# Kernel tuning notes

Measured on AMD Instinct MI355X. Metric: run time of the kernel, lower is better.

The kernel has to match this reference:

```python
import jax, jax.numpy as jnp
import numpy as np

S, T, C, L_GNN, L_TF, H = 8, 16, 128, 3, 2, 4
B = 512
FF = 4 * C
EPS = 1e-5


def setup_inputs() -> dict:
    key = jax.random.key(0)
    ks = jax.random.split(key, 24)
    w = lambda k, shape: jax.random.normal(k, shape, jnp.float32) * 0.05
    inp = {}
    inp["xx"] = jax.random.randint(ks[0], (B, T, S, S, S), 0, 3, dtype=jnp.int32)
    inp["ss"] = jax.random.uniform(ks[1], (B, 1), jnp.float32)
    # DynamicGNNv2 params
    inp["Win"] = w(ks[2], (C, 5)); inp["b_in"] = w(ks[3], (C,))
    inp["Wl"] = w(ks[4], (L_GNN, C, C)); inp["bl"] = w(ks[5], (L_GNN, C))   # SAGEConv lin_l (neighbors)
    inp["Wr"] = w(ks[6], (L_GNN, C, C))                                      # SAGEConv lin_r (root, no bias)
    inp["ln_g"] = jnp.ones((C,), jnp.float32); inp["ln_b"] = jnp.zeros((C,), jnp.float32)  # shared LayerNorm
    # TransformerEncoder params (norm_first, relu, dropout=0 at eval)
    inp["Wqkv"] = w(ks[7], (L_TF, 3 * C, C)); inp["bqkv"] = w(ks[8], (L_TF, 3 * C))
    inp["Wo"] = w(ks[9], (L_TF, C, C)); inp["bo"] = w(ks[10], (L_TF, C))
    inp["ln1_g"] = jnp.ones((L_TF, C), jnp.float32); inp["ln1_b"] = jnp.zeros((L_TF, C), jnp.float32)
    inp["ln2_g"] = jnp.ones((L_TF, C), jnp.float32); inp["ln2_b"] = jnp.zeros((L_TF, C), jnp.float32)
    inp["W1"] = w(ks[11], (L_TF, FF, C)); inp["b1"] = w(ks[12], (L_TF, FF))
    inp["W2"] = w(ks[13], (L_TF, C, FF)); inp["b2"] = w(ks[14], (L_TF, C))
    inp["Wact"] = w(ks[15], (C, S ** 3)); inp["bact"] = w(ks[16], (C,))
    inp["Wsc"] = w(ks[17], (C, 1)); inp["bsc"] = w(ks[18], (C,))
    return inp


def layernorm(x, g, b):
    mu = x.mean(-1, keepdims=True)
    var = ((x - mu) ** 2).mean(-1, keepdims=True)
    return (x - mu) * jax.lax.rsqrt(var + EPS) * g + b


def reference(xx, ss, Win, b_in, Wl, bl, Wr, ln_g, ln_b, Wqkv, bqkv, Wo, bo,
              ln1_g, ln1_b, ln2_g, ln2_b, W1, b1, W2, b2, Wact, bact, Wsc, bsc):
    Bc = xx.shape[0]
    S3 = S ** 3
    frame0 = xx[:, 0].reshape(Bc, S3).astype(jnp.float32)            # (B,S^3)
    m = (frame0 != 0).astype(jnp.float32)                            # active-node mask
    grid = jnp.arange(S3)
    i, j, k = grid // (S * S), (grid // S) % S, grid % S
    coord = jnp.stack([i, j, k], -1).astype(jnp.float32) / (S - 1)   # (S^3,3)
    feat = jnp.concatenate([
        jnp.broadcast_to(coord, (Bc, S3, 3)),
        (frame0 / 2.0)[..., None],
        jnp.broadcast_to((ss / S)[:, None, :], (Bc, S3, 1)),
    ], -1)                                                            # (B,S^3,5)
    x = feat @ Win.T + b_in                                           # lin_in
    mm = m[..., None]
    n = m.sum(-1, keepdims=True)[..., None]                           # nodes per graph (B,1,1)
    for l in range(L_GNN):
        # complete graph (no self loops): mean over neighbors = (sum_active - self)/(N-1)
        s = (x * mm).sum(1, keepdims=True)                            # (B,1,C)
        neigh = jnp.where(n > 1, (s - x) / jnp.maximum(n - 1.0, 1.0), 0.0)
        h = neigh @ Wl[l].T + bl[l] + x @ Wr[l].T                     # SAGEConv
        x = layernorm(jax.nn.relu(h), ln_g, ln_b)
    full = x * mm                                                     # scatter-fill into dense (B,S^3,C)
    # pooling matmul: mean over each i/j/k slice -> (B,3S,C)
    poolW = jnp.concatenate([
        (i[None, :] == jnp.arange(S)[:, None]).astype(jnp.float32),
        (j[None, :] == jnp.arange(S)[:, None]).astype(jnp.float32),
        (k[None, :] == jnp.arange(S)[:, None]).astype(jnp.float32),
    ], 0)                                                             # (3S,S^3)
    gnn_emb = jnp.einsum('ps,bsc->bpc', poolW, full) / poolW.sum(1)[None, :, None]
    # transformer over past actions
    a = xx[:, 1:].reshape(Bc, T - 1, S3).astype(jnp.float32) @ Wact.T + bact
    Hd = C // H
    scale = 1.0 / np.sqrt(Hd).astype(np.float32)
    split_heads = lambda t: t.reshape(Bc, -1, H, Hd).transpose(0, 2, 1, 3)
    for l in range(L_TF):
        h1 = layernorm(a, ln1_g[l], ln1_b[l])
        q, kk, v = jnp.split(h1 @ Wqkv[l].T + bqkv[l], 3, axis=-1)
        q, kk, v = split_heads(q), split_heads(kk), split_heads(v)
        att = jax.nn.softmax(jnp.einsum('bhqd,bhkd->bhqk', q, kk) * scale, -1)
        o = jnp.einsum('bhqk,bhkd->bhqd', att, v).transpose(0, 2, 1, 3).reshape(Bc, -1, C)
        a = a + (o @ Wo[l].T + bo[l])
        h2 = layernorm(a, ln2_g[l], ln2_b[l])
        a = a + (jax.nn.relu(h2 @ W1[l].T + b1[l]) @ W2[l].T + b2[l])
    act_emb = a.mean(1)                                               # (B,C)
    mv_emb = jax.nn.relu(ss @ Wsc.T + bsc)                            # (B,C)
    return jnp.concatenate([gnn_emb, act_emb[:, None], mv_emb[:, None]], 1)  # (B,3S+2,C)
```

## Files before the change

### kernel.cpp

```cpp
#include <hip/hip_runtime.h>
#include <hip/hip_bf16.h>
#include <string.h>

typedef __hip_bfloat16 bf16;
typedef __attribute__((ext_vector_type(8))) short short8;
typedef __attribute__((ext_vector_type(4))) float f32x4;

#define Bsz 512
#define S3  512
#define Tsz 16
#define Cc  128
#define TT  15
#define EPSv 1e-5f

__device__ __forceinline__ float u2f(unsigned short u) {
    return __uint_as_float(((unsigned)u) << 16);
}
__device__ __forceinline__ float ulo(unsigned u) { return __uint_as_float(u << 16); }
__device__ __forceinline__ float uhi(unsigned u) { return __uint_as_float(u & 0xffff0000u); }
__device__ __forceinline__ unsigned short f2bu(float v) {
    bf16 h = __float2bfloat16(v);
    unsigned short u; memcpy(&u, &h, 2); return u;
}
__device__ __forceinline__ unsigned short bfr16(float a) {
    unsigned u = __float_as_uint(a);
    u = u + 0x7fffu + ((u >> 16) & 1u);
    return (unsigned short)(u >> 16);
}
__device__ __forceinline__ unsigned fpack2(float a, float b) {
    unsigned ua = __float_as_uint(a), ub = __float_as_uint(b);
    ua = ua + 0x7fffu + ((ua >> 16) & 1u);
    ub = ub + 0x7fffu + ((ub >> 16) & 1u);
    return (ua >> 16) | (ub & 0xffff0000u);
}
__device__ __forceinline__ float dot4(float4 a, float4 b) {
    return a.x*b.x + a.y*b.y + a.z*b.z + a.w*b.w;
}

__global__ __launch_bounds__(256) void k_tpack(const float* __restrict__ src,
                                               float* __restrict__ dst,
                                               int NR, int NK)
{
    __shared__ float tile[32][33];
    int k0 = blockIdx.x * 32, r0 = blockIdx.y * 32;
    int lr = threadIdx.x >> 5, lk = threadIdx.x & 31;
    for (int i = lr; i < 32; i += 8)
        tile[i][lk] = src[(size_t)(r0 + i) * NK + k0 + lk];
    __syncthreads();
    int c = threadIdx.x & 31, k4 = threadIdx.x >> 5;
    float4 v;
    v.x = tile[c][k4 * 4 + 0]; v.y = tile[c][k4 * 4 + 1];
    v.z = tile[c][k4 * 4 + 2]; v.w = tile[c][k4 * 4 + 3];
    ((float4*)dst)[(size_t)(k0 / 4 + k4) * NR + r0 + c] = v;
}

__global__ __launch_bounds__(256) void k_cvt5(
    const float* __restrict__ s0, const float* __restrict__ s1,
    const float* __restrict__ s2, const float* __restrict__ s3,
    const float* __restrict__ s4, ushort* __restrict__ dst)
{
    int i = blockIdx.x * 256 + threadIdx.x;
    if (i >= 114688) return;
    const float* src; int rel;
    if (i < 16384)      { src = s0; rel = i; }
    else if (i < 40960) { src = s1; rel = i - 16384; }
    else if (i < 49152) { src = s2; rel = i - 40960; }
    else if (i < 81920) { src = s3; rel = i - 49152; }
    else                { src = s4; rel = i - 81920; }
    float4 v = ((const float4*)src)[rel];
    ushort4 o;
    o.x = f2bu(v.x); o.y = f2bu(v.y); o.z = f2bu(v.z); o.w = f2bu(v.w);
    ((ushort4*)dst)[i] = o;
}

__global__ __launch_bounds__(256) void k_dwall(
    const int* __restrict__ xx, const float* __restrict__ Wl,
    const float* __restrict__ Wr, ushort* __restrict__ dbuf)
{
    __shared__ float pc[4];
    __shared__ float winv;
    int b = blockIdx.x, l = blockIdx.y, tid = threadIdx.x;
    const int* x0 = xx + (size_t)b * Tsz * S3;
    int c = (x0[tid] != 0) + (x0[tid + 256] != 0);
    for (int off = 32; off; off >>= 1) c += __shfl_xor(c, off, 64);
    if ((tid & 63) == 0) pc[tid >> 6] = (float)c;
    __syncthreads();
    if (tid == 0) {
        float n = pc[0] + pc[1] + pc[2] + pc[3];
        winv = (n > 1.f) ? 1.f / (n - 1.f) : 0.f;
    }
    __syncthreads();
    float inv = winv;
    const float* wl = Wl + l * 16384;
    const float* wr = Wr + l * 16384;
    ushort* dst = dbuf + (size_t)(b * 3 + l) * 32 * 512;
    for (int item = tid; item < 2048; item += 256) {
        int f = item >> 6, lane = item & 63;
        int t = f >> 2, ks = f & 3, ml = lane & 15, q = lane >> 4;
        int n = t * 16 + ml, kb = ks * 32 + q * 8;
        const float4* wlr = (const float4*)(wl + n * 128 + kb);
        const float4* wrr = (const float4*)(wr + n * 128 + kb);
        float4 a0 = wlr[0], a1 = wlr[1];
        float4 r0 = wrr[0], r1 = wrr[1];
        ushort4 o0, o1;
        o0.x = f2bu(r0.x - inv * a0.x); o0.y = f2bu(r0.y - inv * a0.y);
        o0.z = f2bu(r0.z - inv * a0.z); o0.w = f2bu(r0.w - inv * a0.w);
        o1.x = f2bu(r1.x - inv * a1.x); o1.y = f2bu(r1.y - inv * a1.y);
        o1.z = f2bu(r1.z - inv * a1.z); o1.w = f2bu(r1.w - inv * a1.w);
        ushort* dp = dst + (size_t)f * 512 + lane * 8;
        *(ushort4*)dp = o0;
        *(ushort4*)(dp + 4) = o1;
    }
}

__global__ __launch_bounds__(1024) void k_torso(
    const int* __restrict__ xx, const float* __restrict__ ss,
    const float* __restrict__ Win, const float* __restrict__ b_in,
    const ushort* __restrict__ dbuf,
    const float4* __restrict__ WlP, const float* __restrict__ blv,
    const float* __restrict__ lng, const float* __restrict__ lnb,
    float* __restrict__ out)
{
    __shared__ ushort X[512 * 136];
    __shared__ float  mC[512];
    __shared__ float  sred[16 * 128];
    __shared__ float  ssc[128];
    __shared__ float  sbase[128];
    __shared__ float  gln[128], bln[128];
    __shared__ float  scnt[16];
    __shared__ float  invS;

    int b = blockIdx.x, tid = threadIdx.x;
    int wv = tid >> 6, lane = tid & 63;
    int ml = lane & 15, quad = lane >> 4;

    {
        int g = wv, cp = lane;
        int co0 = 2 * cp, co1 = 2 * cp + 1;
        const int* x0 = xx + (size_t)b * Tsz * S3;
        float f4c = ss[b] * (1.0f / 8.0f);
        float a0 = Win[co0*5+0], a1 = Win[co0*5+1], a2 = Win[co0*5+2], a3 = Win[co0*5+3];
        float c0 = Win[co1*5+0], c1 = Win[co1*5+1], c2 = Win[co1*5+2], c3 = Win[co1*5+3];
        float ba = b_in[co0] + f4c * Win[co0*5+4];
        float bc = b_in[co1] + f4c * Win[co1*5+4];
        float sp0 = 0.f, sp1 = 0.f; int cnt = 0;
        for (int node = g; node < S3; node += 16) {
            int f0 = x0[node];
            float m = (f0 != 0) ? 1.f : 0.f;
            float ci = (float)(node >> 6) * (1.f / 7.f);
            float cj = (float)((node >> 3) & 7) * (1.f / 7.f);
            float ck = (float)(node & 7) * (1.f / 7.f);
            float ft = (float)f0 * 0.5f;
            float v0 = ba + ci * a0 + cj * a1 + ck * a2 + ft * a3;
            float v1 = bc + ci * c0 + cj * c1 + ck * c2 + ft * c3;
            ((unsigned*)(X + node * 136))[cp] = fpack2(v0, v1);
            sp0 += v0 * m; sp1 += v1 * m;
            cnt += (f0 != 0);
            if (cp == 0) mC[node] = m;
        }
        sred[g * 128 + co0] = sp0;
        sred[g * 128 + co1] = sp1;
        if (cp == 0) scnt[g] = (float)cnt;
    }
    if (tid < 128) { gln[tid] = lng[tid]; bln[tid] = lnb[tid]; }
    __syncthreads();
    if (tid == 0) {
        float n = 0.f;
#pragma unroll
        for (int g = 0; g < 16; g++) n += scnt[g];
        invS = (n > 1.f) ? 1.f / (n - 1.f) : 0.f;
    }
    __syncthreads();
    if (tid < 128) {
        float s = 0.f;
#pragma unroll
        for (int g = 0; g < 16; g++) s += sred[g * 128 + tid];
        ssc[tid] = s * invS;
    }
    __syncthreads();
    if (tid < 128) {
        float a = blv[tid];
        for (int k4 = 0; k4 < 32; k4++)
            a += dot4(*(const float4*)(ssc + k4 * 4), WlP[k4 * 384 + tid]);
        sbase[tid] = a;
    }
    __syncthreads();

    for (int l = 0; l < 3; l++) {
        f32x4 acc[8][2];
#pragma unroll
        for (int t = 0; t < 8; t++)
#pragma unroll
            for (int m = 0; m < 2; m++) acc[t][m] = (f32x4){0.f, 0.f, 0.f, 0.f};

        const ushort* dL  = dbuf + (size_t)(b * 3 + l) * 32 * 512 + lane * 8;
        const ushort* xr0 = X + (wv * 32 + ml) * 136 + quad * 8;
        const ushort* xr1 = xr0 + 16 * 136;

#pragma unroll
        for (int ks = 0; ks < 4; ks++) {
            short8 a0 = *(const short8*)(xr0 + ks * 32);
            short8 a1 = *(const short8*)(xr1 + ks * 32);
            short8 bg0[4], bg1[4];
#pragma unroll
            for (int t = 0; t < 4; t++)
                bg0[t] = *(const short8*)(dL + (size_t)(t * 4 + ks) * 512);
#pragma unroll
            for (int t = 0; t < 4; t++)
                bg1[t] = *(const short8*)(dL + (size_t)((t + 4) * 4 + ks) * 512);
#pragma unroll
            for (int t = 0; t < 4; t++) {
                acc[t][0] = __builtin_amdgcn_mfma_f32_16x16x32_bf16(a0, bg0[t], acc[t][0], 0, 0, 0);
                acc[t][1] = __builtin_amdgcn_mfma_f32_16x16x32_bf16(a1, bg0[t], acc[t][1], 0, 0, 0);
            }
#pragma unroll
            for (int t = 0; t < 4; t++) {
                acc[t + 4][0] = __builtin_amdgcn_mfma_f32_16x16x32_bf16(a0, bg1[t], acc[t + 4][0], 0, 0, 0);
                acc[t + 4][1] = __builtin_amdgcn_mfma_f32_16x16x32_bf16(a1, bg1[t], acc[t + 4][1], 0, 0, 0);
            }
        }

        float bse[8], gg[8], be[8];
#pragma unroll
        for (int t = 0; t < 8; t++) {
            bse[t] = sbase[t * 16 + ml];
            gg[t]  = gln[t * 16 + ml];
            be[t]  = bln[t * 16 + ml];
        }
        float sp[8];
#pragma unroll
        for (int t = 0; t < 8; t++) sp[t] = 0.f;
        bool last = (l == 2);

#pragma unroll
        for (int m = 0; m < 2; m++) {
#pragma unroll
            for (int r = 0; r < 4; r++) {
                int row = wv * 32 + m * 16 + quad * 4 + r;
                float s = 0.f, q = 0.f;
#pragma unroll
                for (int t = 0; t < 8; t++) {
                    float v = fmaxf(acc[t][m][r] + bse[t], 0.f);
                    acc[t][m][r] = v;
                    s += v; q += v * v;
                }
#pragma unroll
                for (int off = 1; off <= 8; off <<= 1) {
                    s += __shfl_xor(s, off, 64);
                    q += __shfl_xor(q, off, 64);
                }
                float mu = s * (1.f / 128.f);
                float rs = rsqrtf(q * (1.f / 128.f) - mu * mu + EPSv);
                float mrow = mC[row];
#pragma unroll
                for (int t = 0; t < 8; t++) {
                    float y = (acc[t][m][r] - mu) * rs * gg[t] + be[t];
                    if (last) y *= mrow;
                    else sp[t] += y * mrow;
                    X[row * 136 + t * 16 + ml] = bfr16(y);
                }
            }
        }

        if (!last) {
#pragma unroll
            for (int t = 0; t < 8; t++) {
                sp[t] += __shfl_xor(sp[t], 16, 64);
                sp[t] += __shfl_xor(sp[t], 32, 64);
            }
            if (quad == 0) {
#pragma unroll
                for (int t = 0; t < 8; t++) sred[wv * 128 + t * 16 + ml] = sp[t];
            }
            __syncthreads();
            if (tid < 128) {
                float s = 0.f;
#pragma unroll
                for (int g = 0; g < 16; g++) s += sred[g * 128 + tid];
                ssc[tid] = s * invS;
            }
            __syncthreads();
            if (tid < 128) {
                float a = blv[(l + 1) * 128 + tid];
                for (int k4 = 0; k4 < 32; k4++)
                    a += dot4(*(const float4*)(ssc + k4 * 4), WlP[k4 * 384 + (l + 1) * 128 + tid]);
                sbase[tid] = a;
            }
            __syncthreads();
        }
    }
    __syncthreads();

    if (tid < 768) {
        int c4 = tid & 31, p = tid >> 5;
        int axis = p >> 3, idx = p & 7;
        float4 sum = {0.f, 0.f, 0.f, 0.f};
        for (int t = 0; t < 64; t++) {
            int node;
            if (axis == 0)      node = idx * 64 + t;
            else if (axis == 1) node = (t >> 3) * 64 + idx * 8 + (t & 7);
            else                node = t * 8 + idx;
            uint2 pk = *(const uint2*)(X + node * 136 + c4 * 4);
            sum.x += ulo(pk.x);
            sum.y += uhi(pk.x);
            sum.z += ulo(pk.y);
            sum.w += uhi(pk.y);
        }
        float4 o;
        o.x = sum.x * (1.f / 64.f); o.y = sum.y * (1.f / 64.f);
        o.z = sum.z * (1.f / 64.f); o.w = sum.w * (1.f / 64.f);
        *(float4*)(out + (size_t)b * 26 * Cc + p * Cc + c4 * 4) = o;
    }
}

__global__ __launch_bounds__(256) void k_tf3(
    const int* __restrict__ xx, const float* __restrict__ ss,
    const ushort* __restrict__ WactB, const float* __restrict__ bact,
    const ushort* __restrict__ WqkvB, const float* __restrict__ bqkv,
    const ushort* __restrict__ WoB, const float* __restrict__ bo,
    const float* __restrict__ ln1g, const float* __restrict__ ln1b,
    const float* __restrict__ ln2g, const float* __restrict__ ln2b,
    const ushort* __restrict__ W1B, const float* __restrict__ b1v,
    const ushort* __restrict__ W2B, const float* __restrict__ b2v,
    const float* __restrict__ Wsc, const float* __restrict__ bsc,
    float* __restrict__ out)
{
    __shared__ float  As[TT * 132];
    __shared__ ushort Qs[16 * 392];
    __shared__ ushort Ab[16 * 136];
    __shared__ ushort Hs[16 * 136];
    __shared__ ushort Fs[16 * 520];
    __shared__ float  Att[60 * 16];
    __shared__ float  mu_s[TT], rs_s[TT];

    int b = blockIdx.x, tid = threadIdx.x;
    int wv = tid >> 6, lane = tid & 63;
    int ml = lane & 15, quad = lane >> 4;

    const int* xa = xx + (size_t)b * Tsz * S3 + S3;
    for (int f = tid; f < TT * 512; f += 256) {
        int t = f >> 9, s = f & 511;
        Fs[t * 520 + s] = bfr16((float)xa[t * 512 + s]);
    }
    __syncthreads();

    {
        f32x4 acc[2];
#pragma unroll
        for (int i = 0; i < 2; i++) acc[i] = (f32x4){0.f, 0.f, 0.f, 0.f};
        const ushort* ar = Fs + ml * 520 + quad * 8;
        for (int ks = 0; ks < 16; ks++) {
            short8 a = *(const short8*)(ar + ks * 32);
#pragma unroll
            for (int i = 0; i < 2; i++) {
                int n0 = (wv * 2 + i) * 16;
                short8 bfr = *(const short8*)(WactB + (size_t)(n0 + ml) * 512 + quad * 8 + ks * 32);
                acc[i] = __builtin_amdgcn_mfma_f32_16x16x32_bf16(a, bfr, acc[i], 0, 0, 0);
            }
        }
#pragma unroll
        for (int i = 0; i < 2; i++) {
            int col = (wv * 2 + i) * 16 + ml;
            float bb = bact[col];
#pragma unroll
            for (int r = 0; r < 4; r++) {
                int row = quad * 4 + r;
                if (row < TT) As[row * 132 + col] = acc[i][r] + bb;
            }
        }
    }
    __syncthreads();

    for (int l = 0; l < 2; l++) {
        const float* bq  = bqkv + l * 384;
        const float* bol = bo + l * 128;
        const float* g1  = ln1g + l * 128; const float* be1 = ln1b + l * 128;
        const float* g2  = ln2g + l * 128; const float* be2 = ln2b + l * 128;
        const float* b1l = b1v + l * 512;  const float* b2l = b2v + l * 128;

        for (int r = wv; r < TT; r += 4) {
            float2 v = *(const float2*)(As + r * 132 + lane * 2);
            float s = v.x + v.y, q = v.x * v.x + v.y * v.y;
            for (int off = 32; off; off >>= 1) {
                s += __shfl_xor(s, off, 64);
                q += __shfl_xor(q, off, 64);
            }
            if (lane == 0) {
                float mu = s * (1.f / 128.f);
                mu_s[r] = mu;
                rs_s[r] = rsqrtf(q * (1.f / 128.f) - mu * mu + EPSv);
            }
        }
        __syncthreads();
        for (int f = tid; f < TT * 64; f += 256) {
            int t = f >> 6, cp = f & 63;
            float mu = mu_s[t], rs = rs_s[t];
            float x0 = (As[t * 132 + 2 * cp]     - mu) * rs * g1[2 * cp]     + be1[2 * cp];
            float x1 = (As[t * 132 + 2 * cp + 1] - mu) * rs * g1[2 * cp + 1] + be1[2 * cp + 1];
            ((unsigned*)(Ab + t * 136))[cp] = fpack2(x0, x1);
        }
        __syncthreads();

        {
            short8 a[4];
            const ushort* ar = Ab + ml * 136 + quad * 8;
#pragma unroll
            for (int ks = 0; ks < 4; ks++) a[ks] = *(const short8*)(ar + ks * 32);
#pragma unroll
            for (int i = 0; i < 6; i++) {
                int n0 = (wv * 6 + i) * 16;
                f32x4 acc = (f32x4){0.f, 0.f, 0.f, 0.f};
                const ushort* wb = WqkvB + (size_t)(l * 384 + n0 + ml) * 128 + quad * 8;
#pragma unroll
                for (int ks = 0; ks < 4; ks++) {
                    short8 bfr = *(const short8*)(wb + ks * 32);
                    acc = __builtin_amdgcn_mfma_f32_16x16x32_bf16(a[ks], bfr, acc, 0, 0, 0);
                }
                int col = n0 + ml;
                float bb = bq[col];
#pragma unroll
                for (int r = 0; r < 4; r++) {
                    int row = quad * 4 + r;
                    if (row < TT) Qs[row * 392 + col] = bfr16(acc[r] + bb);
                }
            }
        }
        __syncthreads();

        if (tid < 60) {
            int h = tid / 15, tq = tid % 15;
            const ushort* qp = Qs + tq * 392 + h * 32;
            float sc[TT];
            float mx = -1e30f;
#pragma unroll
            for (int tk = 0; tk < TT; tk++) {
                const ushort* kp = Qs + tk * 392 + 128 + h * 32;
                float d = 0.f;
#pragma unroll
                for (int u = 0; u < 32; u += 4) {
                    uint2 qa = *(const uint2*)(qp + u);
                    uint2 ka = *(const uint2*)(kp + u);
                    d += ulo(qa.x) * ulo(ka.x) + uhi(qa.x) * uhi(ka.x)
                       + ulo(qa.y) * ulo(ka.y) + uhi(qa.y) * uhi(ka.y);
                }
                d *= 0.17677669529663689f;
                sc[tk] = d; mx = fmaxf(mx, d);
            }
            float sum = 0.f;
#pragma unroll
            for (int tk = 0; tk < TT; tk++) { float e = __expf(sc[tk] - mx); sc[tk] = e; sum += e; }
            float r = 1.f / sum;
#pragma unroll
            for (int tk = 0; tk < TT; tk++) Att[tid * 16 + tk] = sc[tk] * r;
        }
        __syncthreads();

        for (int f = tid; f < TT * 64; f += 256) {
            int t = f >> 6, cp = f & 63;
            int h = cp >> 4;
            const float* ap = Att + (h * 15 + t) * 16;
            const ushort* vp = Qs + 256 + 2 * cp;
            float a0 = 0.f, a1 = 0.f;
#pragma unroll
            for (int tk = 0; tk < TT; tk++) {
                float w = ap[tk];
                unsigned pk = *(const unsigned*)(vp + tk * 392);
                a0 += w * ulo(pk);
                a1 += w * uhi(pk);
            }
            ((unsigned*)(Hs + t * 136))[cp] = fpack2(a0, a1);
        }
        __syncthreads();

        {
            short8 a[4];
            const ushort* ar = Hs + ml * 136 + quad * 8;
#pragma unroll
            for (int ks = 0; ks < 4; ks++) a[ks] = *(const short8*)(ar + ks * 32);
#pragma unroll
            for (int i = 0; i < 2; i++) {
                int n0 = (wv * 2 + i) * 16;
                f32x4 acc = (f32x4){0.f, 0.f, 0.f, 0.f};
                const ushort* wb = WoB + (size_t)(l * 128 + n0 + ml) * 128 + quad * 8;
#pragma unroll
                for (int ks = 0; ks < 4; ks++) {
                    short8 bfr = *(const short8*)(wb + ks * 32);
                    acc = __builtin_amdgcn_mfma_f32_16x16x32_bf16(a[ks], bfr, acc, 0, 0, 0);
                }
                int col = n0 + ml;
                float bb = bol[col];
#pragma unroll
                for (int r = 0; r < 4; r++) {
                    int row = quad * 4 + r;
                    if (row < TT) As[row * 132 + col] += acc[r] + bb;
                }
            }
        }
        __syncthreads();

        for (int r = wv; r < TT; r += 4) {
            float2 v = *(const float2*)(As + r * 132 + lane * 2);
            float s = v.x + v.y, q = v.x * v.x + v.y * v.y;
            for (int off = 32; off; off >>= 1) {
                s += __shfl_xor(s, off, 64);
                q += __shfl_xor(q, off, 64);
            }
            if (lane == 0) {
                float mu = s * (1.f / 128.f);
                mu_s[r] = mu;
                rs_s[r] = rsqrtf(q * (1.f / 128.f) - mu * mu + EPSv);
            }
        }
        __syncthreads();
        for (int f = tid; f < TT * 64; f += 256) {
            int t = f >> 6, cp = f & 63;
            float mu = mu_s[t], rs = rs_s[t];
            float x0 = (As[t * 132 + 2 * cp]     - mu) * rs * g2[2 * cp]     + be2[2 * cp];
            float x1 = (As[t * 132 + 2 * cp + 1] - mu) * rs * g2[2 * cp + 1] + be2[2 * cp + 1];
            ((unsigned*)(Ab + t * 136))[cp] = fpack2(x0, x1);
        }
        __syncthreads();

        {
            short8 a[4];
            const ushort* ar = Ab + ml * 136 + quad * 8;
#pragma unroll
            for (int ks = 0; ks < 4; ks++) a[ks] = *(const short8*)(ar + ks * 32);
#pragma unroll
            for (int i = 0; i < 8; i++) {
                int n0 = (wv * 8 + i) * 16;
                f32x4 acc = (f32x4){0.f, 0.f, 0.f, 0.f};
                const ushort* wb = W1B + (size_t)(l * 512 + n0 + ml) * 128 + quad * 8;
#pragma unroll
                for (int ks = 0; ks < 4; ks++) {
                    short8 bfr = *(const short8*)(wb + ks * 32);
                    acc = __builtin_amdgcn_mfma_f32_16x16x32_bf16(a[ks], bfr, acc, 0, 0, 0);
                }
                int col = n0 + ml;
                float bb = b1l[col];
#pragma unroll
                for (int r = 0; r < 4; r++) {
                    int row = quad * 4 + r;
                    if (row < TT) Fs[row * 520 + col] = bfr16(fmaxf(acc[r] + bb, 0.f));
                }
            }
        }
        __syncthreads();

        {
            f32x4 acc[2];
#pragma unroll
            for (int i = 0; i < 2; i++) acc[i] = (f32x4){0.f, 0.f, 0.f, 0.f};
            const ushort* ar = Fs + ml * 520 + quad * 8;
            for (int ks = 0; ks < 16; ks++) {
                short8 a = *(const short8*)(ar + ks * 32);
#pragma unroll
                for (int i = 0; i < 2; i++) {
                    int n0 = (wv * 2 + i) * 16;
                    short8 bfr = *(const short8*)(W2B + (size_t)(l * 128 + n0 + ml) * 512 + quad * 8 + ks * 32);
                    acc[i] = __builtin_amdgcn_mfma_f32_16x16x32_bf16(a, bfr, acc[i], 0, 0, 0);
                }
            }
#pragma unroll
            for (int i = 0; i < 2; i++) {
                int col = (wv * 2 + i) * 16 + ml;
                float bb = b2l[col];
#pragma unroll
                for (int r = 0; r < 4; r++) {
                    int row = quad * 4 + r;
                    if (row < TT) As[row * 132 + col] += acc[i][r] + bb;
                }
            }
        }
        __syncthreads();
    }

    if (tid < 128) {
        float s = 0.f;
#pragma unroll
        for (int t = 0; t < TT; t++) s += As[t * 132 + tid];
        out[(size_t)b * 26 * Cc + 24 * Cc + tid] = s * (1.f / 15.f);
    } else if (tid < 256) {
        int co = tid - 128;
        float v = ss[b] * Wsc[co] + bsc[co];
        out[(size_t)b * 26 * Cc + 25 * Cc + co] = fmaxf(v, 0.f);
    }
}

extern "C" void kernel_launch(void* const* d_in, const int* in_sizes, int n_in,
                              void* d_out, int out_size, void* d_ws, size_t ws_size,
                              hipStream_t stream)
{
    (void)in_sizes; (void)n_in; (void)out_size; (void)ws_size;
    const int*   xx   = (const int*)d_in[0];
    const float* ss   = (const float*)d_in[1];
    const float* Win  = (const float*)d_in[2];
    const float* b_in = (const float*)d_in[3];
    const float* Wl   = (const float*)d_in[4];
    const float* bl   = (const float*)d_in[5];
    const float* Wr   = (const float*)d_in[6];
    const float* lng  = (const float*)d_in[7];
    const float* lnb  = (const float*)d_in[8];
    const float* Wqkv = (const float*)d_in[9];
    const float* bqkv = (const float*)d_in[10];
    const float* Wo   = (const float*)d_in[11];
    const float* bo   = (const float*)d_in[12];
    const float* ln1g = (const float*)d_in[13];
    const float* ln1b = (const float*)d_in[14];
    const float* ln2g = (const float*)d_in[15];
    const float* ln2b = (const float*)d_in[16];
    const float* W1   = (const float*)d_in[17];
    const float* b1   = (const float*)d_in[18];
    const float* W2   = (const float*)d_in[19];
    const float* b2   = (const float*)d_in[20];
    const float* Wact = (const float*)d_in[21];
    const float* bact = (const float*)d_in[22];
    const float* Wsc  = (const float*)d_in[23];
    const float* bsc  = (const float*)d_in[24];
    float* out = (float*)d_out;

    char* ws = (char*)d_ws;
    size_t off = 0;
    float* WlT  = (float*)(ws + off); off += 384 * 128 * 4;
    ushort* dbuf  = (ushort*)(ws + off); off += (size_t)Bsz * 3 * 32 * 512 * 2;
    ushort* WactB = (ushort*)(ws + off); off += 128 * 512 * 2;
    ushort* WqkvB = (ushort*)(ws + off); off += 768 * 128 * 2;
    ushort* WoB   = (ushort*)(ws + off); off += 256 * 128 * 2;
    ushort* W1B   = (ushort*)(ws + off); off += 1024 * 128 * 2;
    ushort* W2B   = (ushort*)(ws + off); off += 256 * 512 * 2;

    k_tpack<<<dim3(4, 12), 256, 0, stream>>>(Wl, WlT, 384, 128);
    k_cvt5<<<448, 256, 0, stream>>>(Wact, Wqkv, Wo, W1, W2, WactB);
    k_dwall<<<dim3(Bsz, 3), 256, 0, stream>>>(xx, Wl, Wr, dbuf);

    k_torso<<<Bsz, 1024, 0, stream>>>(xx, ss, Win, b_in, dbuf,
                                      (const float4*)WlT, bl, lng, lnb, out);

    k_tf3<<<Bsz, 256, 0, stream>>>(xx, ss,
                                   WactB, bact, WqkvB, bqkv, WoB, bo,
                                   ln1g, ln1b, ln2g, ln2b,
                                   W1B, b1, W2B, b2,
                                   Wsc, bsc, out);
}
```

Baseline: 316.4 us.

## Replace per-batch combined GNN weights with shared Wl/Wr and dual MFMA accumulation

Previously a kernel built a per-batch bf16 weight matrix (Wr - inv*Wl) for every batch element and layer, writing and then reading about 50 MB of workspace. Now Wl and Wr are converted to bf16 once in six small blocks. The torso kernel runs two sets of MFMAs (root and neighbor) and combines them in the epilogue as accR - inv*accL. This trades doubled MFMA work and extra accumulator registers for far less global memory traffic and better cache reuse of the small shared weights.

```diff
diff --git a/kernel.cpp b/kernel.cpp
--- a/kernel.cpp
+++ b/kernel.cpp
@@ -13,9 +13,6 @@
 #define TT  15
 #define EPSv 1e-5f
 
-__device__ __forceinline__ float u2f(unsigned short u) {
-    return __uint_as_float(((unsigned)u) << 16);
-}
 __device__ __forceinline__ float ulo(unsigned u) { return __uint_as_float(u << 16); }
 __device__ __forceinline__ float uhi(unsigned u) { return __uint_as_float(u & 0xffff0000u); }
 __device__ __forceinline__ unsigned short f2bu(float v) {
@@ -73,40 +70,22 @@
     ((ushort4*)dst)[i] = o;
 }
 
-__global__ __launch_bounds__(256) void k_dwall(
-    const int* __restrict__ xx, const float* __restrict__ Wl,
-    const float* __restrict__ Wr, ushort* __restrict__ dbuf)
+__global__ __launch_bounds__(256) void k_wgnn(
+    const float* __restrict__ Wl, const float* __restrict__ Wr,
+    ushort* __restrict__ wbuf)
 {
-    __shared__ float pc[4];
-    __shared__ float winv;
-    int b = blockIdx.x, l = blockIdx.y, tid = threadIdx.x;
-    const int* x0 = xx + (size_t)b * Tsz * S3;
-    int c = (x0[tid] != 0) + (x0[tid + 256] != 0);
-    for (int off = 32; off; off >>= 1) c += __shfl_xor(c, off, 64);
-    if ((tid & 63) == 0) pc[tid >> 6] = (float)c;
-    __syncthreads();
-    if (tid == 0) {
-        float n = pc[0] + pc[1] + pc[2] + pc[3];
-        winv = (n > 1.f) ? 1.f / (n - 1.f) : 0.f;
-    }
-    __syncthreads();
-    float inv = winv;
-    const float* wl = Wl + l * 16384;
-    const float* wr = Wr + l * 16384;
-    ushort* dst = dbuf + (size_t)(b * 3 + l) * 32 * 512;
-    for (int item = tid; item < 2048; item += 256) {
+    int bi = blockIdx.x;
+    const float* src = (bi < 3) ? Wl + bi * 16384 : Wr + (bi - 3) * 16384;
+    ushort* dst = wbuf + (size_t)bi * 16384;
+    for (int item = threadIdx.x; item < 2048; item += 256) {
         int f = item >> 6, lane = item & 63;
         int t = f >> 2, ks = f & 3, ml = lane & 15, q = lane >> 4;
         int n = t * 16 + ml, kb = ks * 32 + q * 8;
-        const float4* wlr = (const float4*)(wl + n * 128 + kb);
-        const float4* wrr = (const float4*)(wr + n * 128 + kb);
-        float4 a0 = wlr[0], a1 = wlr[1];
-        float4 r0 = wrr[0], r1 = wrr[1];
+        const float4* wr = (const float4*)(src + n * 128 + kb);
+        float4 v0 = wr[0], v1 = wr[1];
         ushort4 o0, o1;
-        o0.x = f2bu(r0.x - inv * a0.x); o0.y = f2bu(r0.y - inv * a0.y);
-        o0.z = f2bu(r0.z - inv * a0.z); o0.w = f2bu(r0.w - inv * a0.w);
-        o1.x = f2bu(r1.x - inv * a1.x); o1.y = f2bu(r1.y - inv * a1.y);
-        o1.z = f2bu(r1.z - inv * a1.z); o1.w = f2bu(r1.w - inv * a1.w);
+        o0.x = f2bu(v0.x); o0.y = f2bu(v0.y); o0.z = f2bu(v0.z); o0.w = f2bu(v0.w);
+        o1.x = f2bu(v1.x); o1.y = f2bu(v1.y); o1.z = f2bu(v1.z); o1.w = f2bu(v1.w);
         ushort* dp = dst + (size_t)f * 512 + lane * 8;
         *(ushort4*)dp = o0;
         *(ushort4*)(dp + 4) = o1;
@@ -116,7 +95,7 @@
 __global__ __launch_bounds__(1024) void k_torso(
     const int* __restrict__ xx, const float* __restrict__ ss,
     const float* __restrict__ Win, const float* __restrict__ b_in,
-    const ushort* __restrict__ dbuf,
+    const ushort* __restrict__ wbuf,
     const float4* __restrict__ WlP, const float* __restrict__ blv,
     const float* __restrict__ lng, const float* __restrict__ lnb,
     float* __restrict__ out)
@@ -167,14 +146,14 @@
     if (tid == 0) {
         float n = 0.f;
 #pragma unroll
-        for (int g = 0; g < 16; g++) n += scnt[g];
+        for (int k = 0; k < 16; k++) n += scnt[k];
         invS = (n > 1.f) ? 1.f / (n - 1.f) : 0.f;
     }
     __syncthreads();
     if (tid < 128) {
         float s = 0.f;
 #pragma unroll
-        for (int g = 0; g < 16; g++) s += sred[g * 128 + tid];
+        for (int k = 0; k < 16; k++) s += sred[k * 128 + tid];
         ssc[tid] = s * invS;
     }
     __syncthreads();
@@ -186,62 +165,56 @@
     }
     __syncthreads();
 
+    float inv = invS;
     for (int l = 0; l < 3; l++) {
-        f32x4 acc[8][2];
-#pragma unroll
-        for (int t = 0; t < 8; t++)
-#pragma unroll
-            for (int m = 0; m < 2; m++) acc[t][m] = (f32x4){0.f, 0.f, 0.f, 0.f};
-
-        const ushort* dL  = dbuf + (size_t)(b * 3 + l) * 32 * 512 + lane * 8;
-        const ushort* xr0 = X + (wv * 32 + ml) * 136 + quad * 8;
-        const ushort* xr1 = xr0 + 16 * 136;
-
-#pragma unroll
-        for (int ks = 0; ks < 4; ks++) {
-            short8 a0 = *(const short8*)(xr0 + ks * 32);
-            short8 a1 = *(const short8*)(xr1 + ks * 32);
-            short8 bg0[4], bg1[4];
-#pragma unroll
-            for (int t = 0; t < 4; t++)
-                bg0[t] = *(const short8*)(dL + (size_t)(t * 4 + ks) * 512);
-#pragma unroll
-            for (int t = 0; t < 4; t++)
-                bg1[t] = *(const short8*)(dL + (size_t)((t + 4) * 4 + ks) * 512);
-#pragma unroll
-            for (int t = 0; t < 4; t++) {
-                acc[t][0] = __builtin_amdgcn_mfma_f32_16x16x32_bf16(a0, bg0[t], acc[t][0], 0, 0, 0);
-                acc[t][1] = __builtin_amdgcn_mfma_f32_16x16x32_bf16(a1, bg0[t], acc[t][1], 0, 0, 0);
-            }
-#pragma unroll
-            for (int t = 0; t < 4; t++) {
-                acc[t + 4][0] = __builtin_amdgcn_mfma_f32_16x16x32_bf16(a0, bg1[t], acc[t + 4][0], 0, 0, 0);
-                acc[t + 4][1] = __builtin_amdgcn_mfma_f32_16x16x32_bf16(a1, bg1[t], acc[t + 4][1], 0, 0, 0);
-            }
-        }
-
-        float bse[8], gg[8], be[8];
-#pragma unroll
-        for (int t = 0; t < 8; t++) {
-            bse[t] = sbase[t * 16 + ml];
-            gg[t]  = gln[t * 16 + ml];
-            be[t]  = bln[t * 16 + ml];
-        }
+        const ushort* pWl = wbuf + (size_t)l * 16384 + lane * 8;
+        const ushort* pWr = wbuf + (size_t)(l + 3) * 16384 + lane * 8;
+        bool last = (l == 2);
+
         float sp[8];
 #pragma unroll
         for (int t = 0; t < 8; t++) sp[t] = 0.f;
-        bool last = (l == 2);
-
-#pragma unroll
-        for (int m = 0; m < 2; m++) {
+
+#pragma unroll
+        for (int pass = 0; pass < 2; pass++) {
+            int base = wv * 32 + pass * 16;
+
+            f32x4 accR[8], accL[8];
+#pragma unroll
+            for (int t = 0; t < 8; t++) {
+                accR[t] = (f32x4){0.f, 0.f, 0.f, 0.f};
+                accL[t] = (f32x4){0.f, 0.f, 0.f, 0.f};
+            }
+
+            const ushort* xr = X + (base + ml) * 136 + quad * 8;
+#pragma unroll
+            for (int ks = 0; ks < 4; ks++) {
+                short8 a = *(const short8*)(xr + ks * 32);
+#pragma unroll
+                for (int t = 0; t < 8; t++) {
+                    int fo = (t * 4 + ks) * 512;
+                    short8 br = *(const short8*)(pWr + fo);
+                    short8 bl = *(const short8*)(pWl + fo);
+                    accR[t] = __builtin_amdgcn_mfma_f32_16x16x32_bf16(a, br, accR[t], 0, 0, 0);
+                    accL[t] = __builtin_amdgcn_mfma_f32_16x16x32_bf16(a, bl, accL[t], 0, 0, 0);
+                }
+            }
+
+            float bse[8], gg[8], be[8];
+#pragma unroll
+            for (int t = 0; t < 8; t++) {
+                bse[t] = sbase[t * 16 + ml];
+                gg[t]  = gln[t * 16 + ml];
+                be[t]  = bln[t * 16 + ml];
+            }
 #pragma unroll
             for (int r = 0; r < 4; r++) {
-                int row = wv * 32 + m * 16 + quad * 4 + r;
+                int row = base + quad * 4 + r;
                 float s = 0.f, q = 0.f;
 #pragma unroll
                 for (int t = 0; t < 8; t++) {
-                    float v = fmaxf(acc[t][m][r] + bse[t], 0.f);
-                    acc[t][m][r] = v;
+                    float v = fmaxf(accR[t][r] - inv * accL[t][r] + bse[t], 0.f);
+                    accR[t][r] = v;
                     s += v; q += v * v;
                 }
 #pragma unroll
@@ -254,7 +227,7 @@
                 float mrow = mC[row];
 #pragma unroll
                 for (int t = 0; t < 8; t++) {
-                    float y = (acc[t][m][r] - mu) * rs * gg[t] + be[t];
+                    float y = (accR[t][r] - mu) * rs * gg[t] + be[t];
                     if (last) y *= mrow;
                     else sp[t] += y * mrow;
                     X[row * 136 + t * 16 + ml] = bfr16(y);
@@ -276,7 +249,7 @@
             if (tid < 128) {
                 float s = 0.f;
 #pragma unroll
-                for (int g = 0; g < 16; g++) s += sred[g * 128 + tid];
+                for (int k = 0; k < 16; k++) s += sred[k * 128 + tid];
                 ssc[tid] = s * invS;
             }
             __syncthreads();
@@ -621,8 +594,8 @@
 
     char* ws = (char*)d_ws;
     size_t off = 0;
-    float* WlT  = (float*)(ws + off); off += 384 * 128 * 4;
-    ushort* dbuf  = (ushort*)(ws + off); off += (size_t)Bsz * 3 * 32 * 512 * 2;
+    float* WlT   = (float*)(ws + off);  off += 384 * 128 * 4;
+    ushort* wbuf = (ushort*)(ws + off); off += 6 * 16384 * 2;
     ushort* WactB = (ushort*)(ws + off); off += 128 * 512 * 2;
     ushort* WqkvB = (ushort*)(ws + off); off += 768 * 128 * 2;
     ushort* WoB   = (ushort*)(ws + off); off += 256 * 128 * 2;
@@ -631,9 +604,9 @@
 
     k_tpack<<<dim3(4, 12), 256, 0, stream>>>(Wl, WlT, 384, 128);
     k_cvt5<<<448, 256, 0, stream>>>(Wact, Wqkv, Wo, W1, W2, WactB);
-    k_dwall<<<dim3(Bsz, 3), 256, 0, stream>>>(xx, Wl, Wr, dbuf);
-
-    k_torso<<<Bsz, 1024, 0, stream>>>(xx, ss, Win, b_in, dbuf,
+    k_wgnn<<<6, 256, 0, stream>>>(Wl, Wr, wbuf);
+
+    k_torso<<<Bsz, 1024, 0, stream>>>(xx, ss, Win, b_in, wbuf,
                                       (const float4*)WlT, bl, lng, lnb, out);
 
     k_tf3<<<Bsz, 256, 0, stream>>>(xx, ss,
```

Measured after the change: 472.6 us. 1.49x slower.
